# Kernel optimization log

Hardware: AMD Instinct MI355X
Metric: run time of the kernel (lower is better)

## Reference

```python
import jax, jax.numpy as jnp
import numpy as np

P_BINS = 5
T_BINS = 16
B_BINS = P_BINS * T_BINS  # 80
IN_CH = 16
OUT_CH = 32
N_VERTS = 30000   # mesh vertices (cols of conn)
N_PATCH = 30000   # patches (rows of conn / B)
K_NNZ = 3         # nnz per sparse row (interpolation support)


def setup_inputs() -> dict:
    key = jax.random.key(0)
    k1, k2, k3, k4 = jax.random.split(key, 4)
    x = jax.random.normal(k1, (N_VERTS, IN_CH), dtype=jnp.float32)
    conn_idx = jax.random.randint(k2, (N_PATCH * B_BINS, K_NNZ), 0, N_VERTS, dtype=jnp.int32)
    conn_val = jax.random.uniform(k3, (N_PATCH * B_BINS, K_NNZ), dtype=jnp.float32)
    weights = jax.random.normal(k4, (B_BINS, IN_CH, OUT_CH), dtype=jnp.float32)
    return {"x": x, "conn_idx": conn_idx, "conn_val": conn_val, "weights": weights}


def _rotated_weights(weights):
    # layer_weights[j, :, :, i] = weights[(j + p*i) % B]  -> reshape (B*inp, out*t)
    j = jnp.arange(B_BINS)[:, None]
    i = jnp.arange(T_BINS)[None, :]
    idx = (j + P_BINS * i) % B_BINS                       # (B, t)
    lw = weights[idx]                                     # (B, t, inp, out)
    lw = jnp.transpose(lw, (0, 2, 3, 1))                  # (B, inp, out, t)
    return lw.reshape(B_BINS * IN_CH, OUT_CH * T_BINS)


def reference(x, conn_idx, conn_val, weights):
    # sparse.mm(conn, x): gather K vertex features per bin row and weight-sum
    gathered = jnp.einsum('rk,rkc->rc', conn_val, x[conn_idx])  # (N*B, inp)
    h = gathered.reshape(-1, B_BINS * IN_CH)                    # (N, B*inp)
    lw = _rotated_weights(weights)                              # (B*inp, out*t)
    y = h @ lw                                                  # (N, out*t)
    y = y.reshape(-1, OUT_CH, T_BINS)
    return jnp.max(y, axis=-1)                                  # (N, out)
```

## Files before the change

### kernel.cpp

```cpp
#include <hip/hip_runtime.h>
#include <hip/hip_bf16.h>
#include <stdint.h>

#define NP 30000
#define BBINS 80
#define INCH 16
#define OUTCH 32
#define KDIM 1280
#define NDIM 512
#define KSTEPS 40
#define NROWS (NP * BBINS)

typedef __bf16 bf16x8 __attribute__((ext_vector_type(8)));
typedef __bf16 bf16x4 __attribute__((ext_vector_type(4)));
typedef float f32x4 __attribute__((ext_vector_type(4)));

__device__ __forceinline__ void async_ld16(const void* g, void* l) {
    __builtin_amdgcn_global_load_lds(
        (const __attribute__((address_space(1))) unsigned int*)g,
        (__attribute__((address_space(3))) unsigned int*)l,
        16, 0, 0);
}

__global__ void prep_weights(const float* __restrict__ w, __bf16* __restrict__ pw) {
    int gid = blockIdx.x * 256 + threadIdx.x;
    int e  = gid & 7;
    int qs = (gid >> 3) & 3;
    int n  = (gid >> 5) & 511;
    int kc = gid >> 14;
    int kp = kc * 32 + ((qs ^ ((n >> 1) & 3)) << 3) + e;
    int b = kp >> 4, c = kp & 15;
    int o = n >> 4,  t = n & 15;
    int bid = (b + 5 * t) % BBINS;
    pw[gid] = (__bf16)w[(bid * INCH + c) * OUTCH + o];
}

__global__ __launch_bounds__(256) void gather_h(
    const float* __restrict__ x,
    const int*   __restrict__ cidx,
    const float* __restrict__ cval,
    __bf16* __restrict__ h) {
    const int gid = blockIdx.x * 256 + threadIdx.x;
    const int r = gid >> 2;
    const int q = gid & 3;
    const int r3 = r * 3;
    const int i0 = cidx[r3 + 0], i1 = cidx[r3 + 1], i2 = cidx[r3 + 2];
    const float v0 = cval[r3 + 0], v1 = cval[r3 + 1], v2 = cval[r3 + 2];
    const float4 a = *(const float4*)(x + (size_t)i0 * 16 + q * 4);
    const float4 b = *(const float4*)(x + (size_t)i1 * 16 + q * 4);
    const float4 c = *(const float4*)(x + (size_t)i2 * 16 + q * 4);
    bf16x4 hv;
    hv[0] = (__bf16)(v0 * a.x + v1 * b.x + v2 * c.x);
    hv[1] = (__bf16)(v0 * a.y + v1 * b.y + v2 * c.y);
    hv[2] = (__bf16)(v0 * a.z + v1 * b.z + v2 * c.z);
    hv[3] = (__bf16)(v0 * a.w + v1 * b.w + v2 * c.w);
    *(bf16x4*)((char*)h + (size_t)gid * 8) = hv;
}

__global__ __launch_bounds__(256, 2) void gemm_max(
    const __bf16* __restrict__ h,
    const __bf16* __restrict__ pw,
    float* __restrict__ out) {

    __shared__ __align__(16) __bf16 Alds[128 * 32];
    __shared__ __align__(16) __bf16 Blds[256 * 32];

    const int bid = blockIdx.x;
    const int m    = (bid >> 4) * 8 + (bid & 7);
    const int ncol = (bid >> 3) & 1;
    if (m >= 235) return;
    const int mbase = m * 128;

    const int tid  = threadIdx.x;
    const int lane = tid & 63;
    const int wave = tid >> 6;
    const int wave_mrow = wave >> 1;
    const int wave_ncol = wave & 1;

    const int ml = lane & 15, q = lane >> 4;
    const int f = (ml >> 1) & 3;
    int a_off[4], b_off[8];
#pragma unroll
    for (int i = 0; i < 4; ++i)
        a_off[i] = (wave_mrow * 64 + i * 16 + ml) * 64 + ((q ^ f) << 4);
#pragma unroll
    for (int j = 0; j < 8; ++j) {
        int nl = wave_ncol * 128 + j * 16 + ml;
        b_off[j] = nl * 64 + ((q ^ f) << 4);
    }

    f32x4 acc[4][8];
#pragma unroll
    for (int i = 0; i < 4; ++i)
#pragma unroll
        for (int j = 0; j < 8; ++j)
            acc[i][j] = (f32x4){0.f, 0.f, 0.f, 0.f};

    const char* hB  = (const char*)h;
    const char* pwB = (const char*)pw + ncol * 16384 + tid * 16;
    int rg0 = mbase + (tid >> 2);
    int rg1 = rg0 + 64;
    if (rg0 > NP - 1) rg0 = NP - 1;
    if (rg1 > NP - 1) rg1 = NP - 1;
    const int swz = ((tid & 3) ^ ((tid >> 3) & 3)) * 16;
    const char* aSrc0 = hB + (size_t)rg0 * 2560 + swz;
    const char* aSrc1 = hB + (size_t)rg1 * 2560 + swz;
    char* aDst0 = (char*)Alds + tid * 16;
    char* aDst1 = aDst0 + 4096;
    char* bDst  = (char*)Blds + tid * 16;

    for (int kc = 0; kc < KSTEPS; ++kc) {
        const char* bs = pwB + kc * 32768;
#pragma unroll
        for (int i = 0; i < 4; ++i)
            async_ld16(bs + i * 4096, bDst + i * 4096);
        async_ld16(aSrc0 + kc * 64, aDst0);
        async_ld16(aSrc1 + kc * 64, aDst1);
        __syncthreads();

        bf16x8 af[4], bfr[8];
#pragma unroll
        for (int i = 0; i < 4; ++i)
            af[i] = *(const bf16x8*)((const char*)Alds + a_off[i]);
#pragma unroll
        for (int j = 0; j < 8; ++j)
            bfr[j] = *(const bf16x8*)((const char*)Blds + b_off[j]);
#pragma unroll
        for (int i = 0; i < 4; ++i)
#pragma unroll
            for (int j = 0; j < 8; ++j)
                acc[i][j] = __builtin_amdgcn_mfma_f32_16x16x32_bf16(
                    af[i], bfr[j], acc[i][j], 0, 0, 0);
        __syncthreads();
    }

    const int rgrp = lane >> 4;
    const int tl   = lane & 15;
#pragma unroll
    for (int i = 0; i < 4; ++i) {
#pragma unroll
        for (int j = 0; j < 8; ++j) {
            float v0 = acc[i][j][0], v1 = acc[i][j][1];
            float v2 = acc[i][j][2], v3 = acc[i][j][3];
#pragma unroll
            for (int off = 1; off < 16; off <<= 1) {
                v0 = fmaxf(v0, __shfl_xor(v0, off));
                v1 = fmaxf(v1, __shfl_xor(v1, off));
                v2 = fmaxf(v2, __shfl_xor(v2, off));
                v3 = fmaxf(v3, __shfl_xor(v3, off));
            }
            if (tl == 0) {
                const int o  = ncol * 16 + wave_ncol * 8 + j;
                const int pr = mbase + wave_mrow * 64 + i * 16 + rgrp * 4;
                if (pr + 0 < NP) out[(pr + 0) * 32 + o] = v0;
                if (pr + 1 < NP) out[(pr + 1) * 32 + o] = v1;
                if (pr + 2 < NP) out[(pr + 2) * 32 + o] = v2;
                if (pr + 3 < NP) out[(pr + 3) * 32 + o] = v3;
            }
        }
    }
}

extern "C" void kernel_launch(void* const* d_in, const int* in_sizes, int n_in,
                              void* d_out, int out_size, void* d_ws, size_t ws_size,
                              hipStream_t stream) {
    const float* x    = (const float*)d_in[0];
    const int*   cidx = (const int*)d_in[1];
    const float* cval = (const float*)d_in[2];
    const float* w    = (const float*)d_in[3];
    float* out = (float*)d_out;

    __bf16* pw = (__bf16*)d_ws;
    __bf16* h  = (__bf16*)((char*)d_ws + (2 << 20));

    hipLaunchKernelGGL(prep_weights, dim3(2560), dim3(256), 0, stream, w, pw);
    hipLaunchKernelGGL(gather_h, dim3(NROWS * 4 / 256), dim3(256), 0, stream,
                       x, cidx, cval, h);
    hipLaunchKernelGGL(gemm_max, dim3(480), dim3(256), 0, stream,
                       h, (const __bf16*)pw, out);
}
```

Measured before the change: 188.1 us.

## Shrink GEMM M-tile to 64 rows and dedupe gather index loads via shuffles

The GEMM block tile shrinks from 128x256 to 64x256. Each wave now covers all 64 rows and 64 columns, and the grid grows to 938 blocks with a 3-blocks-per-SM occupancy hint, which gives more parallelism and better load balance across CUs. In exchange, each block reuses every B tile load less. In the gather kernel, only one of every four threads loads the index and value triple, then broadcasts it with shuffles, and the loads and stores of h use nontemporal hints to reduce redundant traffic and cache pollution.

```diff
diff --git a/kernel.cpp b/kernel.cpp
--- a/kernel.cpp
+++ b/kernel.cpp
@@ -10,6 +10,7 @@
 #define NDIM 512
 #define KSTEPS 40
 #define NROWS (NP * BBINS)
+#define MTILES 469
 
 typedef __bf16 bf16x8 __attribute__((ext_vector_type(8)));
 typedef __bf16 bf16x4 __attribute__((ext_vector_type(4)));
@@ -40,12 +41,26 @@
     const int*   __restrict__ cidx,
     const float* __restrict__ cval,
     __bf16* __restrict__ h) {
-    const int gid = blockIdx.x * 256 + threadIdx.x;
-    const int r = gid >> 2;
-    const int q = gid & 3;
-    const int r3 = r * 3;
-    const int i0 = cidx[r3 + 0], i1 = cidx[r3 + 1], i2 = cidx[r3 + 2];
-    const float v0 = cval[r3 + 0], v1 = cval[r3 + 1], v2 = cval[r3 + 2];
+    const int gid  = blockIdx.x * 256 + threadIdx.x;
+    const int r    = gid >> 2;
+    const int q    = gid & 3;
+    const int lane = threadIdx.x & 63;
+
+    int i0 = 0, i1 = 0, i2 = 0;
+    float v0 = 0.f, v1 = 0.f, v2 = 0.f;
+    if (q == 0) {
+        const int r3 = r * 3;
+        i0 = __builtin_nontemporal_load(cidx + r3 + 0);
+        i1 = __builtin_nontemporal_load(cidx + r3 + 1);
+        i2 = __builtin_nontemporal_load(cidx + r3 + 2);
+        v0 = __builtin_nontemporal_load(cval + r3 + 0);
+        v1 = __builtin_nontemporal_load(cval + r3 + 1);
+        v2 = __builtin_nontemporal_load(cval + r3 + 2);
+    }
+    const int src = lane & 60;
+    i0 = __shfl(i0, src); i1 = __shfl(i1, src); i2 = __shfl(i2, src);
+    v0 = __shfl(v0, src); v1 = __shfl(v1, src); v2 = __shfl(v2, src);
+
     const float4 a = *(const float4*)(x + (size_t)i0 * 16 + q * 4);
     const float4 b = *(const float4*)(x + (size_t)i1 * 16 + q * 4);
     const float4 c = *(const float4*)(x + (size_t)i2 * 16 + q * 4);
@@ -54,81 +69,76 @@
     hv[1] = (__bf16)(v0 * a.y + v1 * b.y + v2 * c.y);
     hv[2] = (__bf16)(v0 * a.z + v1 * b.z + v2 * c.z);
     hv[3] = (__bf16)(v0 * a.w + v1 * b.w + v2 * c.w);
-    *(bf16x4*)((char*)h + (size_t)gid * 8) = hv;
+    union { bf16x4 h4; unsigned long long u; } cvt;
+    cvt.h4 = hv;
+    __builtin_nontemporal_store(cvt.u,
+        (unsigned long long*)((char*)h + (size_t)gid * 8));
 }
 
-__global__ __launch_bounds__(256, 2) void gemm_max(
+__global__ __launch_bounds__(256, 3) void gemm_max(
     const __bf16* __restrict__ h,
     const __bf16* __restrict__ pw,
     float* __restrict__ out) {
 
-    __shared__ __align__(16) __bf16 Alds[128 * 32];
+    __shared__ __align__(16) __bf16 Alds[64 * 32];
     __shared__ __align__(16) __bf16 Blds[256 * 32];
 
-    const int bid = blockIdx.x;
-    const int m    = (bid >> 4) * 8 + (bid & 7);
-    const int ncol = (bid >> 3) & 1;
-    if (m >= 235) return;
-    const int mbase = m * 128;
+    const int bid  = blockIdx.x;
+    const int mb   = bid >> 1;
+    const int ncol = bid & 1;
+    const int mbase = mb * 64;
 
     const int tid  = threadIdx.x;
     const int lane = tid & 63;
     const int wave = tid >> 6;
-    const int wave_mrow = wave >> 1;
-    const int wave_ncol = wave & 1;
 
     const int ml = lane & 15, q = lane >> 4;
     const int f = (ml >> 1) & 3;
-    int a_off[4], b_off[8];
+    int a_off[4], b_off[4];
 #pragma unroll
     for (int i = 0; i < 4; ++i)
-        a_off[i] = (wave_mrow * 64 + i * 16 + ml) * 64 + ((q ^ f) << 4);
+        a_off[i] = (i * 16 + ml) * 64 + ((q ^ f) << 4);
 #pragma unroll
-    for (int j = 0; j < 8; ++j) {
-        int nl = wave_ncol * 128 + j * 16 + ml;
+    for (int j = 0; j < 4; ++j) {
+        int nl = wave * 64 + j * 16 + ml;
         b_off[j] = nl * 64 + ((q ^ f) << 4);
     }
 
-    f32x4 acc[4][8];
+    f32x4 acc[4][4];
 #pragma unroll
     for (int i = 0; i < 4; ++i)
 #pragma unroll
-        for (int j = 0; j < 8; ++j)
+        for (int j = 0; j < 4; ++j)
             acc[i][j] = (f32x4){0.f, 0.f, 0.f, 0.f};
 
     const char* hB  = (const char*)h;
     const char* pwB = (const char*)pw + ncol * 16384 + tid * 16;
-    int rg0 = mbase + (tid >> 2);
-    int rg1 = rg0 + 64;
-    if (rg0 > NP - 1) rg0 = NP - 1;
-    if (rg1 > NP - 1) rg1 = NP - 1;
+    int rg = mbase + (tid >> 2);
+    if (rg > NP - 1) rg = NP - 1;
     const int swz = ((tid & 3) ^ ((tid >> 3) & 3)) * 16;
-    const char* aSrc0 = hB + (size_t)rg0 * 2560 + swz;
-    const char* aSrc1 = hB + (size_t)rg1 * 2560 + swz;
-    char* aDst0 = (char*)Alds + tid * 16;
-    char* aDst1 = aDst0 + 4096;
-    char* bDst  = (char*)Blds + tid * 16;
+    const char* aSrc = hB + (size_t)rg * 2560 + swz;
+    char* aDst = (char*)Alds + tid * 16;
+    char* bDst = (char*)Blds + tid * 16;
 
     for (int kc = 0; kc < KSTEPS; ++kc) {
         const char* bs = pwB + kc * 32768;
 #pragma unroll
         for (int i = 0; i < 4; ++i)
             async_ld16(bs + i * 4096, bDst + i * 4096);
-        async_ld16(aSrc0 + kc * 64, aDst0);
-        async_ld16(aSrc1 + kc * 64, aDst1);
+        async_ld16(aSrc + kc * 64, aDst);
         __syncthreads();
 
-        bf16x8 af[4], bfr[8];
+        bf16x8 af[4], bfr[4];
 #pragma unroll
         for (int i = 0; i < 4; ++i)
             af[i] = *(const bf16x8*)((const char*)Alds + a_off[i]);
 #pragma unroll
-        for (int j = 0; j < 8; ++j)
+        for (int j = 0; j < 4; ++j)
             bfr[j] = *(const bf16x8*)((const char*)Blds + b_off[j]);
 #pragma unroll
         for (int i = 0; i < 4; ++i)
 #pragma unroll
-            for (int j = 0; j < 8; ++j)
+            for (int j = 0; j < 4; ++j)
                 acc[i][j] = __builtin_amdgcn_mfma_f32_16x16x32_bf16(
                     af[i], bfr[j], acc[i][j], 0, 0, 0);
         __syncthreads();
@@ -139,7 +149,7 @@
 #pragma unroll
     for (int i = 0; i < 4; ++i) {
 #pragma unroll
-        for (int j = 0; j < 8; ++j) {
+        for (int j = 0; j < 4; ++j) {
             float v0 = acc[i][j][0], v1 = acc[i][j][1];
             float v2 = acc[i][j][2], v3 = acc[i][j][3];
 #pragma unroll
@@ -150,8 +160,8 @@
                 v3 = fmaxf(v3, __shfl_xor(v3, off));
             }
             if (tl == 0) {
-                const int o  = ncol * 16 + wave_ncol * 8 + j;
-                const int pr = mbase + wave_mrow * 64 + i * 16 + rgrp * 4;
+                const int o  = ncol * 16 + wave * 4 + j;
+                const int pr = mbase + i * 16 + rgrp * 4;
                 if (pr + 0 < NP) out[(pr + 0) * 32 + o] = v0;
                 if (pr + 1 < NP) out[(pr + 1) * 32 + o] = v1;
                 if (pr + 2 < NP) out[(pr + 2) * 32 + o] = v2;
@@ -176,6 +186,6 @@
     hipLaunchKernelGGL(prep_weights, dim3(2560), dim3(256), 0, stream, w, pw);
     hipLaunchKernelGGL(gather_h, dim3(NROWS * 4 / 256), dim3(256), 0, stream,
                        x, cidx, cval, h);
-    hipLaunchKernelGGL(gemm_max, dim3(480), dim3(256), 0, stream,
+    hipLaunchKernelGGL(gemm_max, dim3(MTILES * 2), dim3(256), 0, stream,
                        h, (const __bf16*)pw, out);
 }
```

Measured after the change: 209.2 us. 11.3% more time.

## Double GEMM k-step depth per barrier and dedupe sparse index loads in gather

Applied to the files above, without the earlier changes.

The GEMM main loop now loads two 32-wide k-slices of A and B into doubled LDS buffers per iteration, halving the number of barrier pairs and the loop trips. The gather kernel has only one lane of each four-lane group load the three indices and weights, with nontemporal hints, and broadcasts them via shuffles, which removes redundant index and value loads. The trade-offs are doubled LDS usage (48 KB per block), which may hurt two-block occupancy, and extra shuffle instructions in the gather.

```diff
diff --git a/kernel.cpp b/kernel.cpp
--- a/kernel.cpp
+++ b/kernel.cpp
@@ -8,7 +8,7 @@
 #define OUTCH 32
 #define KDIM 1280
 #define NDIM 512
-#define KSTEPS 40
+#define KSTEPS2 20
 #define NROWS (NP * BBINS)
 
 typedef __bf16 bf16x8 __attribute__((ext_vector_type(8)));
@@ -40,12 +40,26 @@
     const int*   __restrict__ cidx,
     const float* __restrict__ cval,
     __bf16* __restrict__ h) {
-    const int gid = blockIdx.x * 256 + threadIdx.x;
-    const int r = gid >> 2;
-    const int q = gid & 3;
-    const int r3 = r * 3;
-    const int i0 = cidx[r3 + 0], i1 = cidx[r3 + 1], i2 = cidx[r3 + 2];
-    const float v0 = cval[r3 + 0], v1 = cval[r3 + 1], v2 = cval[r3 + 2];
+    const int gid  = blockIdx.x * 256 + threadIdx.x;
+    const int r    = gid >> 2;
+    const int q    = gid & 3;
+    const int lane = threadIdx.x & 63;
+
+    int i0 = 0, i1 = 0, i2 = 0;
+    float v0 = 0.f, v1 = 0.f, v2 = 0.f;
+    if (q == 0) {
+        const int r3 = r * 3;
+        i0 = __builtin_nontemporal_load(cidx + r3 + 0);
+        i1 = __builtin_nontemporal_load(cidx + r3 + 1);
+        i2 = __builtin_nontemporal_load(cidx + r3 + 2);
+        v0 = __builtin_nontemporal_load(cval + r3 + 0);
+        v1 = __builtin_nontemporal_load(cval + r3 + 1);
+        v2 = __builtin_nontemporal_load(cval + r3 + 2);
+    }
+    const int src = lane & 60;
+    i0 = __shfl(i0, src); i1 = __shfl(i1, src); i2 = __shfl(i2, src);
+    v0 = __shfl(v0, src); v1 = __shfl(v1, src); v2 = __shfl(v2, src);
+
     const float4 a = *(const float4*)(x + (size_t)i0 * 16 + q * 4);
     const float4 b = *(const float4*)(x + (size_t)i1 * 16 + q * 4);
     const float4 c = *(const float4*)(x + (size_t)i2 * 16 + q * 4);
@@ -62,8 +76,8 @@
     const __bf16* __restrict__ pw,
     float* __restrict__ out) {
 
-    __shared__ __align__(16) __bf16 Alds[128 * 32];
-    __shared__ __align__(16) __bf16 Blds[256 * 32];
+    __shared__ __align__(16) __bf16 Alds[2 * 128 * 32];
+    __shared__ __align__(16) __bf16 Blds[2 * 256 * 32];
 
     const int bid = blockIdx.x;
     const int m    = (bid >> 4) * 8 + (bid & 7);
@@ -105,32 +119,41 @@
     const int swz = ((tid & 3) ^ ((tid >> 3) & 3)) * 16;
     const char* aSrc0 = hB + (size_t)rg0 * 2560 + swz;
     const char* aSrc1 = hB + (size_t)rg1 * 2560 + swz;
-    char* aDst0 = (char*)Alds + tid * 16;
-    char* aDst1 = aDst0 + 4096;
-    char* bDst  = (char*)Blds + tid * 16;
-
-    for (int kc = 0; kc < KSTEPS; ++kc) {
-        const char* bs = pwB + kc * 32768;
+    char* aDst = (char*)Alds + tid * 16;
+    char* bDst = (char*)Blds + tid * 16;
+
+    for (int kc = 0; kc < KSTEPS2; ++kc) {
+        const char* bs = pwB + kc * 65536;
 #pragma unroll
         for (int i = 0; i < 4; ++i)
             async_ld16(bs + i * 4096, bDst + i * 4096);
-        async_ld16(aSrc0 + kc * 64, aDst0);
-        async_ld16(aSrc1 + kc * 64, aDst1);
+#pragma unroll
+        for (int i = 0; i < 4; ++i)
+            async_ld16(bs + 32768 + i * 4096, bDst + 16384 + i * 4096);
+        async_ld16(aSrc0 + kc * 128,      aDst);
+        async_ld16(aSrc1 + kc * 128,      aDst + 4096);
+        async_ld16(aSrc0 + kc * 128 + 64, aDst + 8192);
+        async_ld16(aSrc1 + kc * 128 + 64, aDst + 12288);
         __syncthreads();
 
-        bf16x8 af[4], bfr[8];
-#pragma unroll
-        for (int i = 0; i < 4; ++i)
-            af[i] = *(const bf16x8*)((const char*)Alds + a_off[i]);
-#pragma unroll
-        for (int j = 0; j < 8; ++j)
-            bfr[j] = *(const bf16x8*)((const char*)Blds + b_off[j]);
-#pragma unroll
-        for (int i = 0; i < 4; ++i)
+#pragma unroll
+        for (int ks = 0; ks < 2; ++ks) {
+            const char* A = (const char*)Alds + ks * 8192;
+            const char* B = (const char*)Blds + ks * 16384;
+            bf16x8 af[4], bfr[8];
+#pragma unroll
+            for (int i = 0; i < 4; ++i)
+                af[i] = *(const bf16x8*)(A + a_off[i]);
 #pragma unroll
             for (int j = 0; j < 8; ++j)
-                acc[i][j] = __builtin_amdgcn_mfma_f32_16x16x32_bf16(
-                    af[i], bfr[j], acc[i][j], 0, 0, 0);
+                bfr[j] = *(const bf16x8*)(B + b_off[j]);
+#pragma unroll
+            for (int i = 0; i < 4; ++i)
+#pragma unroll
+                for (int j = 0; j < 8; ++j)
+                    acc[i][j] = __builtin_amdgcn_mfma_f32_16x16x32_bf16(
+                        af[i], bfr[j], acc[i][j], 0, 0, 0);
+        }
         __syncthreads();
     }
 
```

Result: no change. 190.1 us (+1.1%).

## Fuse sparse gather into GEMM-max kernel, computing A tile on the fly

Applied to the files above, without the earlier changes.

Removes the separate gather kernel and its bf16 h buffer in global memory. The GEMM kernel now computes each A-tile chunk directly from x, cidx and cval inside the K loop and writes it to LDS. Tiles change to 64 rows by the full 512 columns, so each block loads the entire B slab per K step and no N split is needed. This saves the write and re-read of the intermediate, but puts dependent gather latency inside the MFMA loop without any prefetch of the x loads, and gives a smaller M tile with more B traffic per block.

```diff
diff --git a/kernel.cpp b/kernel.cpp
--- a/kernel.cpp
+++ b/kernel.cpp
@@ -9,10 +9,9 @@
 #define KDIM 1280
 #define NDIM 512
 #define KSTEPS 40
-#define NROWS (NP * BBINS)
+#define MTILES 469
 
 typedef __bf16 bf16x8 __attribute__((ext_vector_type(8)));
-typedef __bf16 bf16x4 __attribute__((ext_vector_type(4)));
 typedef float f32x4 __attribute__((ext_vector_type(4)));
 
 __device__ __forceinline__ void async_ld16(const void* g, void* l) {
@@ -35,57 +34,40 @@
     pw[gid] = (__bf16)w[(bid * INCH + c) * OUTCH + o];
 }
 
-__global__ __launch_bounds__(256) void gather_h(
+__global__ __launch_bounds__(256, 2) void fused_gemm_max(
     const float* __restrict__ x,
     const int*   __restrict__ cidx,
     const float* __restrict__ cval,
-    __bf16* __restrict__ h) {
-    const int gid = blockIdx.x * 256 + threadIdx.x;
-    const int r = gid >> 2;
-    const int q = gid & 3;
-    const int r3 = r * 3;
-    const int i0 = cidx[r3 + 0], i1 = cidx[r3 + 1], i2 = cidx[r3 + 2];
-    const float v0 = cval[r3 + 0], v1 = cval[r3 + 1], v2 = cval[r3 + 2];
-    const float4 a = *(const float4*)(x + (size_t)i0 * 16 + q * 4);
-    const float4 b = *(const float4*)(x + (size_t)i1 * 16 + q * 4);
-    const float4 c = *(const float4*)(x + (size_t)i2 * 16 + q * 4);
-    bf16x4 hv;
-    hv[0] = (__bf16)(v0 * a.x + v1 * b.x + v2 * c.x);
-    hv[1] = (__bf16)(v0 * a.y + v1 * b.y + v2 * c.y);
-    hv[2] = (__bf16)(v0 * a.z + v1 * b.z + v2 * c.z);
-    hv[3] = (__bf16)(v0 * a.w + v1 * b.w + v2 * c.w);
-    *(bf16x4*)((char*)h + (size_t)gid * 8) = hv;
-}
-
-__global__ __launch_bounds__(256, 2) void gemm_max(
-    const __bf16* __restrict__ h,
     const __bf16* __restrict__ pw,
     float* __restrict__ out) {
 
-    __shared__ __align__(16) __bf16 Alds[128 * 32];
-    __shared__ __align__(16) __bf16 Blds[256 * 32];
+    __shared__ __align__(16) __bf16 Alds[64 * 32];
+    __shared__ __align__(16) __bf16 Blds[512 * 32];
 
-    const int bid = blockIdx.x;
-    const int m    = (bid >> 4) * 8 + (bid & 7);
-    const int ncol = (bid >> 3) & 1;
-    if (m >= 235) return;
-    const int mbase = m * 128;
-
+    const int mbase = blockIdx.x * 64;
     const int tid  = threadIdx.x;
     const int lane = tid & 63;
     const int wave = tid >> 6;
-    const int wave_mrow = wave >> 1;
-    const int wave_ncol = wave & 1;
+
+    const int patch_l = tid >> 2;
+    const int chunk   = tid & 3;
+    const int bin_l   = chunk >> 1;
+    const int half    = chunk & 1;
+    int p = mbase + patch_l;
+    if (p > NP - 1) p = NP - 1;
+    const int row0 = p * BBINS + bin_l;
+    char* aW = (char*)Alds + patch_l * 64
+             + ((chunk ^ ((patch_l >> 1) & 3)) << 4);
 
     const int ml = lane & 15, q = lane >> 4;
     const int f = (ml >> 1) & 3;
     int a_off[4], b_off[8];
 #pragma unroll
     for (int i = 0; i < 4; ++i)
-        a_off[i] = (wave_mrow * 64 + i * 16 + ml) * 64 + ((q ^ f) << 4);
+        a_off[i] = (i * 16 + ml) * 64 + ((q ^ f) << 4);
 #pragma unroll
     for (int j = 0; j < 8; ++j) {
-        int nl = wave_ncol * 128 + j * 16 + ml;
+        int nl = wave * 128 + j * 16 + ml;
         b_off[j] = nl * 64 + ((q ^ f) << 4);
     }
 
@@ -96,26 +78,41 @@
         for (int j = 0; j < 8; ++j)
             acc[i][j] = (f32x4){0.f, 0.f, 0.f, 0.f};
 
-    const char* hB  = (const char*)h;
-    const char* pwB = (const char*)pw + ncol * 16384 + tid * 16;
-    int rg0 = mbase + (tid >> 2);
-    int rg1 = rg0 + 64;
-    if (rg0 > NP - 1) rg0 = NP - 1;
-    if (rg1 > NP - 1) rg1 = NP - 1;
-    const int swz = ((tid & 3) ^ ((tid >> 3) & 3)) * 16;
-    const char* aSrc0 = hB + (size_t)rg0 * 2560 + swz;
-    const char* aSrc1 = hB + (size_t)rg1 * 2560 + swz;
-    char* aDst0 = (char*)Alds + tid * 16;
-    char* aDst1 = aDst0 + 4096;
-    char* bDst  = (char*)Blds + tid * 16;
+    const char* pwB = (const char*)pw + tid * 16;
+    char* bDst = (char*)Blds + tid * 16;
+
+    int r3 = row0 * 3;
+    int i0 = cidx[r3], i1 = cidx[r3 + 1], i2 = cidx[r3 + 2];
+    float v0 = cval[r3], v1 = cval[r3 + 1], v2 = cval[r3 + 2];
 
     for (int kc = 0; kc < KSTEPS; ++kc) {
         const char* bs = pwB + kc * 32768;
 #pragma unroll
-        for (int i = 0; i < 4; ++i)
+        for (int i = 0; i < 8; ++i)
             async_ld16(bs + i * 4096, bDst + i * 4096);
-        async_ld16(aSrc0 + kc * 64, aDst0);
-        async_ld16(aSrc1 + kc * 64, aDst1);
+
+        const float* xp0 = x + (size_t)(unsigned)i0 * 16 + half * 8;
+        const float* xp1 = x + (size_t)(unsigned)i1 * 16 + half * 8;
+        const float* xp2 = x + (size_t)(unsigned)i2 * 16 + half * 8;
+        const float4 a0 = *(const float4*)xp0, a1 = *(const float4*)(xp0 + 4);
+        const float4 b0 = *(const float4*)xp1, b1 = *(const float4*)(xp1 + 4);
+        const float4 c0 = *(const float4*)xp2, c1 = *(const float4*)(xp2 + 4);
+        bf16x8 hv;
+        hv[0] = (__bf16)(v0 * a0.x + v1 * b0.x + v2 * c0.x);
+        hv[1] = (__bf16)(v0 * a0.y + v1 * b0.y + v2 * c0.y);
+        hv[2] = (__bf16)(v0 * a0.z + v1 * b0.z + v2 * c0.z);
+        hv[3] = (__bf16)(v0 * a0.w + v1 * b0.w + v2 * c0.w);
+        hv[4] = (__bf16)(v0 * a1.x + v1 * b1.x + v2 * c1.x);
+        hv[5] = (__bf16)(v0 * a1.y + v1 * b1.y + v2 * c1.y);
+        hv[6] = (__bf16)(v0 * a1.z + v1 * b1.z + v2 * c1.z);
+        hv[7] = (__bf16)(v0 * a1.w + v1 * b1.w + v2 * c1.w);
+        *(bf16x8*)aW = hv;
+
+        if (kc + 1 < KSTEPS) {
+            r3 = (row0 + (kc + 1) * 2) * 3;
+            i0 = cidx[r3]; i1 = cidx[r3 + 1]; i2 = cidx[r3 + 2];
+            v0 = cval[r3]; v1 = cval[r3 + 1]; v2 = cval[r3 + 2];
+        }
         __syncthreads();
 
         bf16x8 af[4], bfr[8];
@@ -140,22 +137,22 @@
     for (int i = 0; i < 4; ++i) {
 #pragma unroll
         for (int j = 0; j < 8; ++j) {
-            float v0 = acc[i][j][0], v1 = acc[i][j][1];
-            float v2 = acc[i][j][2], v3 = acc[i][j][3];
+            float v0r = acc[i][j][0], v1r = acc[i][j][1];
+            float v2r = acc[i][j][2], v3r = acc[i][j][3];
 #pragma unroll
             for (int off = 1; off < 16; off <<= 1) {
-                v0 = fmaxf(v0, __shfl_xor(v0, off));
-                v1 = fmaxf(v1, __shfl_xor(v1, off));
-                v2 = fmaxf(v2, __shfl_xor(v2, off));
-                v3 = fmaxf(v3, __shfl_xor(v3, off));
+                v0r = fmaxf(v0r, __shfl_xor(v0r, off));
+                v1r = fmaxf(v1r, __shfl_xor(v1r, off));
+                v2r = fmaxf(v2r, __shfl_xor(v2r, off));
+                v3r = fmaxf(v3r, __shfl_xor(v3r, off));
             }
             if (tl == 0) {
-                const int o  = ncol * 16 + wave_ncol * 8 + j;
-                const int pr = mbase + wave_mrow * 64 + i * 16 + rgrp * 4;
-                if (pr + 0 < NP) out[(pr + 0) * 32 + o] = v0;
-                if (pr + 1 < NP) out[(pr + 1) * 32 + o] = v1;
-                if (pr + 2 < NP) out[(pr + 2) * 32 + o] = v2;
-                if (pr + 3 < NP) out[(pr + 3) * 32 + o] = v3;
+                const int o  = wave * 8 + j;
+                const int pr = mbase + i * 16 + rgrp * 4;
+                if (pr + 0 < NP) out[(pr + 0) * 32 + o] = v0r;
+                if (pr + 1 < NP) out[(pr + 1) * 32 + o] = v1r;
+                if (pr + 2 < NP) out[(pr + 2) * 32 + o] = v2r;
+                if (pr + 3 < NP) out[(pr + 3) * 32 + o] = v3r;
             }
         }
     }
@@ -171,11 +168,8 @@
     float* out = (float*)d_out;
 
     __bf16* pw = (__bf16*)d_ws;
-    __bf16* h  = (__bf16*)((char*)d_ws + (2 << 20));
 
     hipLaunchKernelGGL(prep_weights, dim3(2560), dim3(256), 0, stream, w, pw);
-    hipLaunchKernelGGL(gather_h, dim3(NROWS * 4 / 256), dim3(256), 0, stream,
-                       x, cidx, cval, h);
-    hipLaunchKernelGGL(gemm_max, dim3(480), dim3(256), 0, stream,
-                       h, (const __bf16*)pw, out);
+    hipLaunchKernelGGL(fused_gemm_max, dim3(MTILES), dim3(256), 0, stream,
+                       x, cidx, cval, (const __bf16*)pw, out);
 }
```

After: 192.3 us. 2.3% more time.
